# Kernel tuning notes

Measured on AMD Instinct MI355X. Metric: run time of the kernel, lower is better.

Reference implementation:

```python
import jax, jax.numpy as jnp
import numpy as np

D = 256        # controller_lstm_size
BR = 8         # child_branch_num
UNITS = 12     # child_unit_num
TEMP = 5.0
TANHC = 1.1
MAXA = UNITS + 2   # max number of anchors
NEG = -1e9


def setup_inputs() -> dict:
    key = jax.random.key(0)
    ks = jax.random.split(key, 9)
    u = lambda k, s: jax.random.uniform(k, s, jnp.float32, -0.1, 0.1)
    # b_soft: zeros with first two entries = 10, excluded from uniform init
    b_soft = jnp.zeros((BR,), jnp.float32).at[:2].set(10.0)
    return {
        "encoder": u(ks[0], (BR + 1, D)),   # nn.Embedding(branch_num+1, D)
        "W_ih": u(ks[1], (4 * D, D)),       # LSTMCell weight_ih (i,f,g,o)
        "W_hh": u(ks[2], (4 * D, D)),
        "b_ih": u(ks[3], (4 * D,)),
        "b_hh": u(ks[4], (4 * D,)),
        "w_soft": u(ks[5], (BR, D)),
        "b_soft": b_soft,
        "w_attn_1": u(ks[6], (D, D)),
        "w_attn_2": u(ks[7], (D, D)),
        "v_attn": u(ks[8], (D,)),
    }


def _sample(key, logits):
    """Categorical sample + NLL(cross_entropy) + entropy term (batch-1)."""
    idx = jax.random.categorical(key, jax.lax.stop_gradient(logits))
    logp = jax.nn.log_softmax(logits)
    ent = -jnp.sum(jax.nn.softmax(logits) * logp)
    return idx, -logp[idx], ent


def _run_sampler(p, key, c0, h0, use_bias):
    b_no_learn = jnp.asarray([0.25, 0.25] + [-0.25] * (BR - 2), jnp.float32)

    def lstm(x, h, c):
        g = x @ p["W_ih"].T + p["b_ih"] + h @ p["W_hh"].T + p["b_hh"]
        i, f, gc, o = jnp.split(g, 4, axis=-1)
        c2 = jax.nn.sigmoid(f) * c + jax.nn.sigmoid(i) * jnp.tanh(gc)
        return jax.nn.sigmoid(o) * jnp.tanh(c2), c2

    anchors = jnp.zeros((MAXA, D), jnp.float32)
    anchors_w1 = jnp.zeros((MAXA, D), jnp.float32)
    h, c = h0, c0
    x = p["encoder"][0]
    for i in range(2):  # two seed units, anchors stay zero
        h, c = lstm(x, h, c)
        anchors_w1 = anchors_w1.at[i].set(p["w_attn_1"] @ h)

    def step(carry, unit_id):
        h, c, x, anchors, anchors_w1, key, lp, ent = carry
        mask = jnp.arange(MAXA) < unit_id
        idxs, ops = [], []
        for _ in range(2):  # sample two input indices via attention
            h, c = lstm(x, h, c)
            q = jnp.tanh(anchors_w1 + p["w_attn_2"] @ h)     # [MAXA, D]
            logits = q @ p["v_attn"]                          # [MAXA]
            logits = TANHC * jnp.tanh(logits / TEMP)
            logits = jnp.where(mask, logits, NEG)
            key, sub = jax.random.split(key)
            idx, nll, e = _sample(sub, logits)
            lp = lp + nll
            ent = ent + jax.lax.stop_gradient(e)
            x = anchors[idx]
            idxs.append(idx)
        for _ in range(2):  # sample two ops
            h, c = lstm(x, h, c)
            logits = p["w_soft"] @ h + p["b_soft"]
            logits = TANHC * jnp.tanh(logits / TEMP)
            if use_bias:
                logits = logits + b_no_learn
            key, sub = jax.random.split(key)
            op, nll, e = _sample(sub, logits)
            lp = lp + nll
            ent = ent + jax.lax.stop_gradient(e)
            x = p["encoder"][op + 1]
            ops.append(op)
        h, c = lstm(x, h, c)  # final step adds a new anchor
        anchors = anchors.at[unit_id].set(h)
        anchors_w1 = anchors_w1.at[unit_id].set(p["w_attn_1"] @ h)
        x = p["encoder"][0]
        out = jnp.stack([idxs[0], ops[0], idxs[1], ops[1]])  # [idx1,op1,idx2,op2]
        return (h, c, x, anchors, anchors_w1, key, lp, ent), out

    z = jnp.float32(0.0)
    init = (h, c, x, anchors, anchors_w1, key, z, z)
    (h, c, *_rest, lp, ent), arcs = jax.lax.scan(
        step, init, jnp.arange(2, UNITS + 2))
    return arcs.reshape(-1), ent, lp, c, h


def reference(encoder, W_ih, W_hh, b_ih, b_hh, w_soft, b_soft,
              w_attn_1, w_attn_2, v_attn):
    p = {"encoder": encoder, "W_ih": W_ih, "W_hh": W_hh, "b_ih": b_ih,
         "b_hh": b_hh, "w_soft": w_soft, "b_soft": b_soft,
         "w_attn_1": w_attn_1, "w_attn_2": w_attn_2, "v_attn": v_attn}
    k1, k2 = jax.random.split(jax.random.key(123))
    z = jnp.zeros((D,), jnp.float32)
    arc1, e1, l1, c, h = _run_sampler(p, k1, z, z, use_bias=True)
    arc2, e2, l2, _, _ = _run_sampler(p, k2, c, h, use_bias=False)
    return arc1, arc2, l1 + l2, e1 + e2
```

## Files before the change

### kernel.cpp

```cpp
#include <hip/hip_runtime.h>
#include <cstdint>

#define D     256
#define NB    32
#define TPB   256
#define HS    8
#define NROW  32
#define MAXA  14
#define UNITS 12
#define NEGV  (-1e9f)

__device__ unsigned long long g_Hq[2 * D];
__device__ unsigned long long g_PartQ[2 * NB*16];

__global__ void init_kernel() {
  int i = threadIdx.x;
  if (i < 2 * D) g_Hq[i] = 0ull;
  if (i < 2 * NB * 16) g_PartQ[i] = 0ull;
}

__device__ __forceinline__ void qstore(unsigned long long* p, unsigned gen,
                                       float v) {
  unsigned long long q =
      ((unsigned long long)gen << 32) | (unsigned long long)__float_as_uint(v);
  __hip_atomic_store(p, q, __ATOMIC_RELAXED, __HIP_MEMORY_SCOPE_AGENT);
}

__device__ __forceinline__ float qpoll(unsigned long long* p, unsigned gen) {
  unsigned long long q;
  long spins = 0;
  for (;;) {
    q = __hip_atomic_load(p, __ATOMIC_RELAXED, __HIP_MEMORY_SCOPE_AGENT);
    if ((unsigned)(q >> 32) == gen) break;
    __builtin_amdgcn_s_sleep(1);
    if (++spins > 20000000L) break;
  }
  return __uint_as_float((unsigned)q);
}

__device__ __forceinline__ uint32_t rotl32(uint32_t v, uint32_t n) {
  return (v << n) | (v >> (32u - n));
}

__device__ uint2 tf2x32(uint2 k, uint32_t x0, uint32_t x1) {
  uint32_t ks0 = k.x, ks1 = k.y, ks2 = 0x1BD11BDAu ^ ks0 ^ ks1;
  x0 += ks0; x1 += ks1;
#define TF4(a,b,c,d) \
  x0 += x1; x1 = rotl32(x1,(a)); x1 ^= x0; \
  x0 += x1; x1 = rotl32(x1,(b)); x1 ^= x0; \
  x0 += x1; x1 = rotl32(x1,(c)); x1 ^= x0; \
  x0 += x1; x1 = rotl32(x1,(d)); x1 ^= x0;
  TF4(13,15,26,6)  x0 += ks1; x1 += ks2 + 1u;
  TF4(17,29,16,24) x0 += ks2; x1 += ks0 + 2u;
  TF4(13,15,26,6)  x0 += ks0; x1 += ks1 + 3u;
  TF4(17,29,16,24) x0 += ks1; x1 += ks2 + 4u;
  TF4(13,15,26,6)  x0 += ks2; x1 += ks0 + 5u;
#undef TF4
  return make_uint2(x0, x1);
}

__device__ __forceinline__ float gumbelf(uint32_t bits) {
  float f = __uint_as_float((bits >> 9) | 0x3f800000u) - 1.0f;
  const float tiny = 1.17549435082228751e-38f;
  float u = fmaxf(tiny, f);
  return -logf(-logf(u));
}

__device__ __forceinline__ float sigm(float x) {
  return 0.5f + 0.5f * tanhf(0.5f * x);
}

__global__ void __launch_bounds__(TPB) ENAScontroller_21706764714567_kernel(
    const float* __restrict__ enc,   const float* __restrict__ Wih,
    const float* __restrict__ Whh,   const float* __restrict__ bih,
    const float* __restrict__ bhh,   const float* __restrict__ wsoft,
    const float* __restrict__ bsoft, const float* __restrict__ wa1,
    const float* __restrict__ wa2,   const float* __restrict__ vattn,
    float* __restrict__ out)
{
  const int b    = blockIdx.x;
  const int t    = threadIdx.x;
  const int lane = t & 63;
  const int wv_  = t >> 6;

  unsigned hgen = 0;
  unsigned pgen = 0;

  __shared__ float4 sWhh4[64 * NROW];
  __shared__ float4 sWa1p[64 * HS];
  __shared__ float4 sWa2p[64 * HS];
  __shared__ __align__(16) float s_h[D];
  __shared__ float s_part[TPB];
  __shared__ float s_pp[NB * 16];
  __shared__ float s_eW[9][NROW];
  __shared__ float s_aW[MAXA][NROW];
  __shared__ float s_aw1[MAXA][HS];
  __shared__ float s_t2[HS];
  __shared__ float s_vs[HS];
  __shared__ float s_c[HS];
  __shared__ float s_bc[NROW];
  __shared__ float s_bsoft[8];
  __shared__ float s_log[16];
  __shared__ float s_z[16];
  __shared__ uint2 s_pair[2];
  __shared__ uint2 s_key;
  __shared__ int   s_sel;
  __shared__ float s_lp, s_ent;

  for (int idx = t; idx < 64 * NROW; idx += TPB) {
    int kk = idx >> 5, j = idx & 31;
    int grow = (j >> 3) * D + b * HS + (j & 7);
    sWhh4[idx] = *(const float4*)&Whh[grow * D + kk * 4];
  }
  for (int idx = t; idx < 64 * HS; idx += TPB) {
    int kk = idx >> 3, j = idx & 7;
    sWa1p[idx] = *(const float4*)&wa1[(b * HS + j) * D + kk * 4];
    sWa2p[idx] = *(const float4*)&wa2[(b * HS + j) * D + kk * 4];
  }
  if (t < NROW) {
    int grow = (t >> 3) * D + b * HS + (t & 7);
    s_bc[t] = bih[grow] + bhh[grow];
  }
  if (t < HS) {
    s_vs[t] = vattn[b * HS + t];
    s_c[t] = 0.f;
  }
  if (t < 8) s_bsoft[t] = bsoft[t];
  s_h[t] = 0.f;
  if (t == 0) { s_lp = 0.f; s_ent = 0.f; }
  if (t < 2) s_pair[t] = tf2x32(make_uint2(0u, 123u), 0u, (uint32_t)t);
  __syncthreads();
  const uint2 key1 = s_pair[0];
  const uint2 key2 = s_pair[1];

  for (int m = 0; m < 8; ++m) {
    int j = wv_ * 8 + m;
    int grow = wv_ * D + b * HS + m;
    float4 wrow = *(const float4*)&Wih[grow * D + lane * 4];
    for (int r = 0; r < 9; ++r) {
      float4 ev = *(const float4*)&enc[r * D + lane * 4];
      float x = wrow.x * ev.x + wrow.y * ev.y + wrow.z * ev.z + wrow.w * ev.w;
      #pragma unroll
      for (int s = 32; s; s >>= 1) x += __shfl_xor(x, s);
      if (lane == 0) s_eW[r][j] = x;
    }
  }
  __syncthreads();

  auto LSTM_PRE = [&](const float* xd) {
    {
      int j = t & 31, p = t >> 5;
      const float4* hp = (const float4*)s_h;
      float acc = 0.f;
      #pragma unroll
      for (int q = 0; q < 8; ++q) {
        int kk = p * 8 + q;
        float4 wvv = sWhh4[kk * 32 + j];
        float4 hv  = hp[kk];
        acc += wvv.x * hv.x + wvv.y * hv.y + wvv.z * hv.z + wvv.w * hv.w;
      }
      s_part[t] = acc;
    }
    __syncthreads();
    ++hgen;
    if (t < HS) {
      float gg[4];
      #pragma unroll
      for (int q = 0; q < 4; ++q) {
        int j = q * 8 + t;
        float s = s_bc[j] + xd[j];
        #pragma unroll
        for (int p = 0; p < 8; ++p) s += s_part[p * 32 + j];
        gg[q] = s;
      }
      float c2 = sigm(gg[1]) * s_c[t] + sigm(gg[0]) * tanhf(gg[2]);
      float hn = sigm(gg[3]) * tanhf(c2);
      s_c[t] = c2;
      qstore(&g_Hq[(hgen & 1) * D + b * HS + t], hgen, hn);
    }
  };

  auto LSTM_POST = [&]() {
    __syncthreads();
    float hv = qpoll(&g_Hq[(hgen & 1) * D + t], hgen);
    s_h[t] = hv;
    __syncthreads();
  };

  auto DOT8 = [&](const float4* M, float* dst) {
    if (t < 64) {
      int j = t & 7, p = t >> 3;
      const float4* hp = (const float4*)s_h;
      float acc = 0.f;
      #pragma unroll
      for (int q = 0; q < 8; ++q) {
        int kk = p * 8 + q;
        float4 m4 = M[kk * 8 + j];
        float4 hv = hp[kk];
        acc += m4.x * hv.x + m4.y * hv.y + m4.z * hv.z + m4.w * hv.w;
      }
      s_part[t] = acc;
    }
    __syncthreads();
    if (t < 8) {
      float s = 0.f;
      #pragma unroll
      for (int p = 0; p < 8; ++p) s += s_part[p * 8 + t];
      dst[t] = s;
    }
    __syncthreads();
  };

  auto AWC = [&](int slot) {
    const float4* hp = (const float4*)s_h;
    for (int m = 0; m < 8; ++m) {
      int j = wv_ * 8 + m;
      int grow = wv_ * D + b * HS + m;
      float4 wrow = *(const float4*)&Wih[grow * D + lane * 4];
      float4 hv = hp[lane];
      float x = wrow.x * hv.x + wrow.y * hv.y + wrow.z * hv.z + wrow.w * hv.w;
      #pragma unroll
      for (int s = 32; s; s >>= 1) x += __shfl_xor(x, s);
      if (lane == 0) s_aW[slot][j] = x;
    }
    __syncthreads();
  };

  auto ATTN = [&]() {
    DOT8(sWa2p, s_t2);
    ++pgen;
    if (t < MAXA) {
      float pa = 0.f;
      #pragma unroll
      for (int d2 = 0; d2 < HS; ++d2)
        pa += tanhf(s_aw1[t][d2] + s_t2[d2]) * s_vs[d2];
      qstore(&g_PartQ[(pgen & 1) * (NB * 16) + b * 16 + t], pgen, pa);
    }
    {
      unsigned long long* base2 = &g_PartQ[(pgen & 1) * (NB * 16)];
      #pragma unroll
      for (int s = t; s < NB * 16; s += TPB)
        if ((s & 15) < MAXA) s_pp[s] = qpoll(&base2[s], pgen);
    }
    __syncthreads();
  };

  auto ALOGITS = [&](int u) {
    if (t < MAXA) {
      float l = 0.f;
      #pragma unroll
      for (int bb = 0; bb < NB; ++bb) l += s_pp[bb * 16 + t];
      l = 1.1f * tanhf(l / 5.0f);
      s_log[t] = (t < u) ? l : NEGV;
    }
    __syncthreads();
  };

  auto OLOGITS = [&](bool useBias) {
    if (t < 64) {
      int j = t & 7, p = t >> 3;
      const float4* hp = (const float4*)s_h;
      float acc = 0.f;
      #pragma unroll
      for (int q = 0; q < 8; ++q) {
        int kk = p * 8 + q;
        float4 m4 = *(const float4*)&wsoft[j * D + kk * 4];
        float4 hv = hp[kk];
        acc += m4.x * hv.x + m4.y * hv.y + m4.z * hv.z + m4.w * hv.w;
      }
      s_part[t] = acc;
    }
    __syncthreads();
    if (t < 8) {
      float s = 0.f;
      #pragma unroll
      for (int p = 0; p < 8; ++p) s += s_part[p * 8 + t];
      float l = s + s_bsoft[t];
      l = 1.1f * tanhf(l / 5.0f);
      if (useBias) l += (t < 2 ? 0.25f : -0.25f);
      s_log[t] = l;
    }
    __syncthreads();
  };

  auto SAMPLE = [&](int N) -> int {
    if (t < 2) s_pair[t] = tf2x32(s_key, 0u, (uint32_t)t);
    __syncthreads();
    uint2 sub = s_pair[1];
    if (t == 0) s_key = s_pair[0];
    if (t < N) {
      uint2 e = tf2x32(sub, 0u, (uint32_t)t);
      s_z[t] = s_log[t] + gumbelf(e.x ^ e.y);
    }
    __syncthreads();
    if (t == 0) {
      int bi = 0; float bz = s_z[0];
      for (int a = 1; a < N; ++a) if (s_z[a] > bz) { bz = s_z[a]; bi = a; }
      float m = s_log[0];
      for (int a = 1; a < N; ++a) m = fmaxf(m, s_log[a]);
      float ssum = 0.f, sdl = 0.f;
      for (int a = 0; a < N; ++a) {
        float d2 = s_log[a] - m;
        float e2 = expf(d2);
        ssum += e2; sdl += e2 * d2;
      }
      float ls = logf(ssum);
      s_lp  += -(s_log[bi] - m - ls);
      s_ent += ls - sdl / ssum;
      s_sel = bi;
    }
    __syncthreads();
    return s_sel;
  };

  for (int smp = 0; smp < 2; ++smp) {
    for (int idx = t; idx < MAXA * NROW; idx += TPB) (&s_aW[0][0])[idx]  = 0.f;
    for (int idx = t; idx < MAXA * HS;   idx += TPB) (&s_aw1[0][0])[idx] = 0.f;
    if (t == 0) s_key = (smp == 0) ? key1 : key2;
    __syncthreads();

    LSTM_PRE(s_eW[0]);
    LSTM_POST();
    LSTM_PRE(s_eW[0]);
    DOT8(sWa1p, s_aw1[0]);
    LSTM_POST();

    bool useBias = (smp == 0);
    for (int u = 2; u < 2 + UNITS; ++u) {
      LSTM_PRE(s_eW[0]);
      DOT8(sWa1p, s_aw1[u - 1]);
      if (u > 2) AWC(u - 1);
      LSTM_POST();

      ATTN(); ALOGITS(u);
      int i1 = SAMPLE(MAXA);
      LSTM_PRE(s_aW[i1]); LSTM_POST();

      ATTN(); ALOGITS(u);
      int i2 = SAMPLE(MAXA);
      LSTM_PRE(s_aW[i2]); LSTM_POST();

      OLOGITS(useBias);
      int o1 = SAMPLE(8);
      LSTM_PRE(s_eW[o1 + 1]); LSTM_POST();

      OLOGITS(useBias);
      int o2 = SAMPLE(8);
      LSTM_PRE(s_eW[o2 + 1]); LSTM_POST();

      if (b == 0 && t == 0) {
        int base = smp * 48 + (u - 2) * 4;
        out[base + 0] = (float)i1;
        out[base + 1] = (float)o1;
        out[base + 2] = (float)i2;
        out[base + 3] = (float)o2;
      }
    }
  }
  if (b == 0 && t == 0) {
    out[96] = s_lp;
    out[97] = s_ent;
  }
}

extern "C" __attribute__((visibility("default")))
void kernel_launch(void* const* d_in, const int* in_sizes, int n_in,
                   void* d_out, int out_size, void* d_ws, size_t ws_size,
                   hipStream_t stream) {
  const float* enc   = (const float*)d_in[0];
  const float* Wih   = (const float*)d_in[1];
  const float* Whh   = (const float*)d_in[2];
  const float* bih   = (const float*)d_in[3];
  const float* bhh   = (const float*)d_in[4];
  const float* wsoft = (const float*)d_in[5];
  const float* bsoft = (const float*)d_in[6];
  const float* wa1   = (const float*)d_in[7];
  const float* wa2   = (const float*)d_in[8];
  const float* vattn = (const float*)d_in[9];
  float* out = (float*)d_out;

  init_kernel<<<dim3(1), dim3(1024), 0, stream>>>();
  ENAScontroller_21706764714567_kernel<<<dim3(NB), dim3(TPB), 0, stream>>>(
      enc, Wih, Whh, bih, bhh, wsoft, bsoft, wa1, wa2, vattn, out);
}
```

Baseline: 590.1 us.

## Overlap recurrent W_hh matvec with cross-block attention gather and sampling

Splits the LSTM step into a W_hh·h matvec and a gate-update phase. The matvec depends only on the current hidden state, not on the sampled input, so it now runs while the kernel waits on the cross-block attention partial-sum gather and before sampling. The goal is to take the matvec and one barrier off the serial critical path between global polls. It adds a separate shared-memory buffer so the matvec result is not overwritten by other phases, and it relies on the matvec output surviving until the gates consume it.

Measured after the change: 567.3 us. 1.04x faster.

```diff
diff --git a/kernel.cpp b/kernel.cpp
--- a/kernel.cpp
+++ b/kernel.cpp
@@ -91,6 +91,7 @@
   __shared__ float4 sWa2p[64 * HS];
   __shared__ __align__(16) float s_h[D];
   __shared__ float s_part[TPB];
+  __shared__ float s_mv[TPB];
   __shared__ float s_pp[NB * 16];
   __shared__ float s_eW[9][NROW];
   __shared__ float s_aW[MAXA][NROW];
@@ -147,21 +148,22 @@
   }
   __syncthreads();
 
-  auto LSTM_PRE = [&](const float* xd) {
-    {
-      int j = t & 31, p = t >> 5;
-      const float4* hp = (const float4*)s_h;
-      float acc = 0.f;
-      #pragma unroll
-      for (int q = 0; q < 8; ++q) {
-        int kk = p * 8 + q;
-        float4 wvv = sWhh4[kk * 32 + j];
-        float4 hv  = hp[kk];
-        acc += wvv.x * hv.x + wvv.y * hv.y + wvv.z * hv.z + wvv.w * hv.w;
-      }
-      s_part[t] = acc;
-    }
-    __syncthreads();
+  auto MATVEC = [&]() {
+    int j = t & 31, p = t >> 5;
+    const float4* hp = (const float4*)s_h;
+    float acc = 0.f;
+    #pragma unroll
+    for (int q = 0; q < 8; ++q) {
+      int kk = p * 8 + q;
+      float4 wvv = sWhh4[kk * 32 + j];
+      float4 hv  = hp[kk];
+      acc += wvv.x * hv.x + wvv.y * hv.y + wvv.z * hv.z + wvv.w * hv.w;
+    }
+    s_mv[t] = acc;
+    __syncthreads();
+  };
+
+  auto GATES = [&](const float* xd) {
     ++hgen;
     if (t < HS) {
       float gg[4];
@@ -170,7 +172,7 @@
         int j = q * 8 + t;
         float s = s_bc[j] + xd[j];
         #pragma unroll
-        for (int p = 0; p < 8; ++p) s += s_part[p * 32 + j];
+        for (int p = 0; p < 8; ++p) s += s_mv[p * 32 + j];
         gg[q] = s;
       }
       float c2 = sigm(gg[1]) * s_c[t] + sigm(gg[0]) * tanhf(gg[2]);
@@ -226,8 +228,7 @@
     __syncthreads();
   };
 
-  auto ATTN = [&]() {
-    DOT8(sWa2p, s_t2);
+  auto PSTORE = [&]() {
     ++pgen;
     if (t < MAXA) {
       float pa = 0.f;
@@ -236,12 +237,13 @@
         pa += tanhf(s_aw1[t][d2] + s_t2[d2]) * s_vs[d2];
       qstore(&g_PartQ[(pgen & 1) * (NB * 16) + b * 16 + t], pgen, pa);
     }
-    {
-      unsigned long long* base2 = &g_PartQ[(pgen & 1) * (NB * 16)];
-      #pragma unroll
-      for (int s = t; s < NB * 16; s += TPB)
-        if ((s & 15) < MAXA) s_pp[s] = qpoll(&base2[s], pgen);
-    }
+  };
+
+  auto PGATHER = [&]() {
+    unsigned long long* base2 = &g_PartQ[(pgen & 1) * (NB * 16)];
+    #pragma unroll
+    for (int s = t; s < NB * 16; s += TPB)
+      if ((s & 15) < MAXA) s_pp[s] = qpoll(&base2[s], pgen);
     __syncthreads();
   };
 
@@ -319,34 +321,46 @@
     if (t == 0) s_key = (smp == 0) ? key1 : key2;
     __syncthreads();
 
-    LSTM_PRE(s_eW[0]);
+    MATVEC(); GATES(s_eW[0]);
     LSTM_POST();
-    LSTM_PRE(s_eW[0]);
+    MATVEC(); GATES(s_eW[0]);
     DOT8(sWa1p, s_aw1[0]);
     LSTM_POST();
 
     bool useBias = (smp == 0);
     for (int u = 2; u < 2 + UNITS; ++u) {
-      LSTM_PRE(s_eW[0]);
+      MATVEC(); GATES(s_eW[0]);
       DOT8(sWa1p, s_aw1[u - 1]);
       if (u > 2) AWC(u - 1);
       LSTM_POST();
 
-      ATTN(); ALOGITS(u);
+      DOT8(sWa2p, s_t2);
+      PSTORE();
+      MATVEC();
+      PGATHER(); ALOGITS(u);
       int i1 = SAMPLE(MAXA);
-      LSTM_PRE(s_aW[i1]); LSTM_POST();
-
-      ATTN(); ALOGITS(u);
+      GATES(s_aW[i1]);
+      LSTM_POST();
+
+      DOT8(sWa2p, s_t2);
+      PSTORE();
+      MATVEC();
+      PGATHER(); ALOGITS(u);
       int i2 = SAMPLE(MAXA);
-      LSTM_PRE(s_aW[i2]); LSTM_POST();
+      GATES(s_aW[i2]);
+      LSTM_POST();
 
       OLOGITS(useBias);
+      MATVEC();
       int o1 = SAMPLE(8);
-      LSTM_PRE(s_eW[o1 + 1]); LSTM_POST();
+      GATES(s_eW[o1 + 1]);
+      LSTM_POST();
 
       OLOGITS(useBias);
+      MATVEC();
       int o2 = SAMPLE(8);
-      LSTM_PRE(s_eW[o2 + 1]); LSTM_POST();
+      GATES(s_eW[o2 + 1]);
+      LSTM_POST();
 
       if (b == 0 && t == 0) {
         int base = smp * 48 + (u - 2) * 4;
```
